# Kernel tuning notes

Measured on AMD Instinct MI355X. Metric: run time of the kernel, lower is better.

The kernel has to match this reference:

```python
import jax, jax.numpy as jnp
import numpy as np


def setup_inputs() -> dict:
    key = jax.random.key(0)
    k0, k1, k2, k3 = jax.random.split(key, 4)
    B, in_dim, n_vars, out_dim, E = 64, 512, 512, 720, 8
    x = jax.random.normal(k0, (B, in_dim, n_vars), dtype=jnp.float32)
    # Gating: nn.Linear(in_dim, E, bias=False) -> weight [E, in_dim]
    Wg = jax.random.normal(k1, (E, in_dim), dtype=jnp.float32) * 0.02
    # Experts: nn.Linear(in_dim, out_dim) -> weight [out_dim, in_dim], bias [out_dim]
    We = jax.random.normal(k2, (E, out_dim, in_dim), dtype=jnp.float32) * 0.02
    be = jax.random.normal(k3, (E, out_dim), dtype=jnp.float32) * 0.02
    return {"x": x, "Wg": Wg, "We": We, "be": be, "top_k": 2}


def reference(x, Wg, We, be, top_k):
    # x: [B, in_len, n_vars] -> tokens along n_vars with feature dim in_len
    xt = jnp.swapaxes(x, 1, 2)                      # [B, V, D]
    gate = jax.nn.softmax(xt @ Wg.T, axis=-1)       # [B, V, E]
    weights, sel = jax.lax.top_k(gate, top_k)       # [B, V, k]
    E, O, D = We.shape
    out = jnp.zeros(xt.shape[:2] + (O,), dtype=xt.dtype)  # [B, V, O]
    for e in range(E):
        # combine weight for expert e: sum over top-k slots routed to e
        coef = jnp.sum(jnp.where(sel == e, weights, jnp.zeros_like(weights)), axis=-1)  # [B, V]
        out = out + coef[..., None] * (jnp.einsum('bvd,od->bvo', xt, We[e]) + be[e])
    return jnp.swapaxes(out, 1, 2)                  # [B, pred_len, n_vars]
```

## Files before the change

### kernel.cpp

```cpp
#include <hip/hip_runtime.h>
#include <hip/hip_bf16.h>

#define DID 512
#define NV  512
#define NB  64
#define OD  720
#define OPAD 768
#define NE  8
#define NTOK (NB * NV)
#define MAXTILE 512

typedef short  bf16x8 __attribute__((ext_vector_type(8)));
typedef float  f32x4  __attribute__((ext_vector_type(4)));

#define XT_OFF    0u
#define WB_OFF    33554432u
#define PID_OFF   39845888u
#define C1D_OFF   39976960u
#define C2D_OFF   40108032u
#define TL_OFF    40239104u
#define CL1_OFF   40370176u
#define CL2_OFF   40501248u
#define BCNT_OFF  40632320u
#define BFILL_OFF 40632576u
#define BOFF_OFF  40632832u
#define TPID_OFF  40633088u
#define TT0_OFF   40635136u
#define TEND_OFF  40637184u
#define NT_OFF    40639232u
#define SCR_OFF   40639488u
#define SCR_END   87825408u

static __device__ __forceinline__ ushort f2bf(float f) {
  unsigned u = __float_as_uint(f);
  unsigned r = (u + 0x7fffu + ((u >> 16) & 1u)) >> 16;
  return (ushort)r;
}
static __device__ __forceinline__ float bf2f(ushort u) {
  return __uint_as_float(((unsigned)u) << 16);
}
static __device__ __forceinline__ void async16(const ushort* g, ushort* l) {
  __builtin_amdgcn_global_load_lds((__attribute__((address_space(1))) void*)(g),
                                   (__attribute__((address_space(3))) void*)(l),
                                   16, 0, 0);
}
static __device__ __forceinline__ int swz(int r) { return (r & 3) ^ ((r >> 2) & 1); }

__global__ __launch_bounds__(512) void k_gatet_wb(const float* __restrict__ x,
                                                  const float* __restrict__ Wg,
                                                  const float* __restrict__ We,
                                                  ushort* __restrict__ xt,
                                                  ushort* __restrict__ wb,
                                                  int* __restrict__ pairid,
                                                  float* __restrict__ c1d,
                                                  float* __restrict__ c2d,
                                                  int* __restrict__ bcnt) {
  const int bid = blockIdx.x;
  const int tid = threadIdx.x;

  if (bid >= 512) {
    const int idx = (bid - 512) * 512 + tid;
    const int e = idx / (OPAD * DID);
    const int r = idx - e * (OPAD * DID);
    const int o = r >> 9;
    ushort val = 0;
    if (o < OD) val = f2bf(We[(size_t)e * OD * DID + r]);
    wb[(size_t)e * OPAD * DID + idx - e * (OPAD * DID)] = val;
    return;
  }

  __shared__ float wg[NE * DID];
  __shared__ float part[8][64][NE + 1];
  __shared__ int cnt64[64];
  for (int i = tid; i < NE * DID / 4; i += 512)
    ((float4*)wg)[i] = ((const float4*)Wg)[i];
  if (tid < 64) cnt64[tid] = 0;
  __syncthreads();

  const int b    = bid >> 3;
  const int v0   = (bid & 7) * 64;
  const int w    = tid >> 6;
  const int lane = tid & 63;
  const int v    = v0 + lane;
  const int d0   = w * 64;
  const float* xp = x + ((size_t)b * DID + d0) * NV + v;
  ushort* xtp = xt + ((size_t)b * NV + v) * DID + d0;

  float acc[NE];
#pragma unroll
  for (int e = 0; e < NE; ++e) acc[e] = 0.f;

  for (int c = 0; c < 64; c += 8) {
    float xv[8];
#pragma unroll
    for (int u = 0; u < 8; ++u) xv[u] = xp[(size_t)(c + u) * NV];
#pragma unroll
    for (int e = 0; e < NE; ++e) {
      const float* wp = &wg[e * DID + d0 + c];
      float4 wa = *(const float4*)wp;
      float4 wb4 = *(const float4*)(wp + 4);
      acc[e] += xv[0] * wa.x + xv[1] * wa.y + xv[2] * wa.z + xv[3] * wa.w
              + xv[4] * wb4.x + xv[5] * wb4.y + xv[6] * wb4.z + xv[7] * wb4.w;
    }
    bf16x8 pk;
#pragma unroll
    for (int u = 0; u < 8; ++u) pk[u] = (short)f2bf(xv[u]);
    *(bf16x8*)(xtp + c) = pk;
  }

#pragma unroll
  for (int e = 0; e < NE; ++e) part[w][lane][e] = acc[e];
  __syncthreads();

  if (tid < 64) {
    float a[NE];
#pragma unroll
    for (int e = 0; e < NE; ++e) {
      float s = part[0][tid][e];
#pragma unroll
      for (int q = 1; q < 8; ++q) s += part[q][tid][e];
      a[e] = s;
    }
    float mx = a[0];
#pragma unroll
    for (int e = 1; e < NE; ++e) mx = fmaxf(mx, a[e]);
    float sum = 0.f;
#pragma unroll
    for (int e = 0; e < NE; ++e) { a[e] = __expf(a[e] - mx); sum += a[e]; }
    const float inv = 1.f / sum;

    int i1 = 0; float g1 = a[0];
#pragma unroll
    for (int e = 1; e < NE; ++e) if (a[e] > g1) { g1 = a[e]; i1 = e; }
    int i2 = -1; float g2 = -1.f;
#pragma unroll
    for (int e = 0; e < NE; ++e) if (e != i1 && a[e] > g2) { g2 = a[e]; i2 = e; }
    g1 *= inv; g2 *= inv;

    int ea, eb; float ca, cb;
    if (i1 < i2) { ea = i1; eb = i2; ca = g1; cb = g2; }
    else         { ea = i2; eb = i1; ca = g2; cb = g1; }
    const int pid = ea * 8 + eb;
    const int t = b * NV + v0 + tid;
    pairid[t] = pid; c1d[t] = ca; c2d[t] = cb;
    atomicAdd(&cnt64[pid], 1);
  }
  __syncthreads();
  if (tid < 64 && cnt64[tid]) atomicAdd(&bcnt[tid], cnt64[tid]);
}

__global__ __launch_bounds__(256) void k_scatter(const int* __restrict__ pairid,
                                                 const float* __restrict__ c1d,
                                                 const float* __restrict__ c2d,
                                                 const int* __restrict__ bcnt,
                                                 int* __restrict__ bfill,
                                                 int* __restrict__ tlist,
                                                 float* __restrict__ cl1,
                                                 float* __restrict__ cl2,
                                                 int* __restrict__ tpid,
                                                 int* __restrict__ tt0,
                                                 int* __restrict__ tend,
                                                 int* __restrict__ ntp) {
  __shared__ int cnt64[64], base64[64], boffl[64];
  const int tid = threadIdx.x;
  if (tid < 64) {
    const int c = bcnt[tid];
    int run = c;
#pragma unroll
    for (int s = 1; s < 64; s <<= 1) {
      int up = __shfl_up(run, s, 64);
      if (tid >= s) run += up;
    }
    const int excl = run - c;
    boffl[tid] = excl;
    cnt64[tid] = 0;
    if (blockIdx.x == 0) {
      const int ntiles = (c + 127) >> 7;
      int trun = ntiles;
#pragma unroll
      for (int s = 1; s < 64; s <<= 1) {
        int up = __shfl_up(trun, s, 64);
        if (tid >= s) trun += up;
      }
      const int texcl = trun - ntiles;
      for (int i = 0; i < ntiles; ++i) {
        tpid[texcl + i] = tid;
        tt0[texcl + i]  = excl + i * 128;
        tend[texcl + i] = run;
      }
      if (tid == 63) ntp[0] = trun;
    }
  }
  __syncthreads();
  const int t = blockIdx.x * 256 + tid;
  const int pid = pairid[t];
  const int p = atomicAdd(&cnt64[pid], 1);
  __syncthreads();
  if (tid < 64) base64[tid] = cnt64[tid] ? atomicAdd(&bfill[tid], cnt64[tid]) : 0;
  __syncthreads();
  const int slot = boffl[pid] + base64[pid] + p;
  tlist[slot] = t; cl1[slot] = c1d[t]; cl2[slot] = c2d[t];
}

__global__ __launch_bounds__(256, 2) void k_gemm(
    const ushort* __restrict__ xt, const ushort* __restrict__ wb,
    const float* __restrict__ be, const int* __restrict__ tlist,
    const float* __restrict__ cl1, const float* __restrict__ cl2,
    const int* __restrict__ tpid, const int* __restrict__ tt0,
    const int* __restrict__ tendarr, const int* __restrict__ ntp,
    ushort* __restrict__ scratch, float* __restrict__ out, int mode) {
  const int tile = blockIdx.x;
  if (tile >= ntp[0]) return;
  const int pid  = tpid[tile];
  const int t0   = tt0[tile];
  const int tend = tendarr[tile];
  const int e1 = pid >> 3, e2 = pid & 7;
  const int o0 = blockIdx.y * 256;

  __shared__ __align__(16) ushort As[3][8192];
  __shared__ __align__(16) ushort Bs[3][4096];

  const int tid  = threadIdx.x;
  const int lane = tid & 63;
  const int w    = tid >> 6;

  int aoffA[4];
#pragma unroll
  for (int i = 0; i < 4; ++i) {
    const int f = w * 256 + i * 64 + lane;
    const int r = f >> 2, p = f & 3, q = p ^ swz(r);
    aoffA[i] = (o0 + r) * DID + q * 8;
  }
  int boffB[2];
#pragma unroll
  for (int i = 0; i < 2; ++i) {
    const int f = w * 128 + i * 64 + lane;
    const int r = f >> 2, p = f & 3, q = p ^ swz(r);
    const int sl = t0 + r;
    const int tk = (sl < tend) ? tlist[sl] : 0;
    boffB[i] = tk * DID + q * 8;
  }

  const int m    = lane & 15;
  const int quad = lane >> 4;
  const int wt   = (w & 1) * 64;
  const int wo   = (w >> 1) * 128;

  float ratio[4], c2v[4]; int tokv[4]; bool gv[4];
#pragma unroll
  for (int j = 0; j < 4; ++j) {
    const int sl = t0 + wt + j * 16 + m;
    gv[j] = sl < tend;
    const float cc1 = gv[j] ? cl1[sl] : 0.f;
    const float cc2 = gv[j] ? cl2[sl] : 1.f;
    ratio[j] = cc1 / cc2;
    c2v[j]   = gv[j] ? cc2 : 0.f;
    tokv[j]  = gv[j] ? tlist[sl] : 0;
  }

  f32x4 acc[8][4];
#pragma unroll
  for (int i = 0; i < 8; ++i)
#pragma unroll
    for (int j = 0; j < 4; ++j) acc[i][j] = (f32x4){0.f, 0.f, 0.f, 0.f};

#define STAGE(t, buf) do {                                          \
    const int eA_ = ((t) < 16) ? e1 : e2;                           \
    const int k0_ = ((t) & 15) * 32;                                \
    const ushort* wA_ = wb + (size_t)eA_ * OPAD * DID + k0_;        \
    async16(wA_ + aoffA[0], &As[buf][w * 2048]);                    \
    async16(wA_ + aoffA[1], &As[buf][w * 2048 + 512]);              \
    async16(wA_ + aoffA[2], &As[buf][w * 2048 + 1024]);             \
    async16(wA_ + aoffA[3], &As[buf][w * 2048 + 1536]);             \
    async16(xt + boffB[0] + k0_, &Bs[buf][w * 1024]);               \
    async16(xt + boffB[1] + k0_, &Bs[buf][w * 1024 + 512]);         \
  } while (0)

#define FRAGS(buf)                                                       \
    bf16x8 af[8], bfr[4];                                                \
    {                                                                    \
      const ushort* Asb = &As[buf][0];                                   \
      const ushort* Bsb = &Bs[buf][0];                                   \
      _Pragma("unroll")                                                  \
      for (int i = 0; i < 8; ++i) {                                      \
        const int R = wo + i * 16 + m;                                   \
        af[i] = *(const bf16x8*)(Asb + R * 32 + ((quad ^ swz(R)) << 3)); \
      }                                                                  \
      _Pragma("unroll")                                                  \
      for (int j = 0; j < 4; ++j) {                                      \
        const int R = wt + j * 16 + m;                                   \
        bfr[j] = *(const bf16x8*)(Bsb + R * 32 + ((quad ^ swz(R)) << 3));\
      }                                                                  \
    }

#define MFMA32()                                                         \
    __builtin_amdgcn_s_setprio(1);                                       \
    _Pragma("unroll")                                                    \
    for (int i = 0; i < 8; ++i)                                          \
      _Pragma("unroll")                                                  \
      for (int j = 0; j < 4; ++j)                                        \
        acc[i][j] = __builtin_amdgcn_mfma_f32_16x16x32_bf16(af[i], bfr[j],\
                                                            acc[i][j], 0, 0, 0); \
    __builtin_amdgcn_s_setprio(0);

  STAGE(0, 0);
  STAGE(1, 1);

  int cur = 0;
  int st  = 2;
  for (int kk = 0; kk < 30; ++kk) {
    asm volatile("s_waitcnt vmcnt(6)" ::: "memory");
    __builtin_amdgcn_s_barrier();
    if (kk == 16) {
      const float* be1p = be + e1 * OD;
#pragma unroll
      for (int i = 0; i < 8; ++i) {
        const int ob = o0 + wo + i * 16 + quad * 4;
        float b0 = 0, b1 = 0, b2 = 0, b3 = 0;
        if (ob < OD) { b0 = be1p[ob]; b1 = be1p[ob + 1]; b2 = be1p[ob + 2]; b3 = be1p[ob + 3]; }
#pragma unroll
        for (int j = 0; j < 4; ++j) {
          acc[i][j][0] = (acc[i][j][0] + b0) * ratio[j];
          acc[i][j][1] = (acc[i][j][1] + b1) * ratio[j];
          acc[i][j][2] = (acc[i][j][2] + b2) * ratio[j];
          acc[i][j][3] = (acc[i][j][3] + b3) * ratio[j];
        }
      }
    }

    STAGE(kk + 2, st);
    FRAGS(cur)
    MFMA32()
    cur = (cur == 2) ? 0 : cur + 1;
    st  = (st  == 2) ? 0 : st  + 1;
  }

  {
    asm volatile("s_waitcnt vmcnt(6)" ::: "memory");
    __builtin_amdgcn_s_barrier();
    FRAGS(0)
    MFMA32()
  }
  {
    asm volatile("s_waitcnt vmcnt(0)" ::: "memory");
    __builtin_amdgcn_s_barrier();
    FRAGS(1)
    MFMA32()
  }

#undef STAGE
#undef FRAGS
#undef MFMA32

  const float* be2p = be + e2 * OD;
#pragma unroll
  for (int i = 0; i < 8; ++i) {
    const int ob = o0 + wo + i * 16 + quad * 4;
    if (ob < OD) {
      const float b0 = be2p[ob], b1 = be2p[ob + 1], b2 = be2p[ob + 2], b3 = be2p[ob + 3];
#pragma unroll
      for (int j = 0; j < 4; ++j) {
        if (gv[j]) {
          const float v0 = c2v[j] * (acc[i][j][0] + b0);
          const float v1 = c2v[j] * (acc[i][j][1] + b1);
          const float v2 = c2v[j] * (acc[i][j][2] + b2);
          const float v3 = c2v[j] * (acc[i][j][3] + b3);
          if (mode == 0) {
            ushort4 pk = make_ushort4(f2bf(v0), f2bf(v1), f2bf(v2), f2bf(v3));
            *(ushort4*)(scratch + (size_t)tokv[j] * OD + ob) = pk;
          } else {
            const int bb = tokv[j] >> 9, vv = tokv[j] & 511;
            float* op = out + ((size_t)bb * OD + ob) * NV + vv;
            op[0] = v0; op[(size_t)NV] = v1; op[2 * (size_t)NV] = v2; op[3 * (size_t)NV] = v3;
          }
        }
      }
    }
  }
}

__global__ __launch_bounds__(256) void k_combine(const ushort* __restrict__ scratch,
                                                 float* __restrict__ out) {
  __shared__ ushort s[64][68];
  const int v0 = blockIdx.x * 64;
  const int o0 = blockIdx.y * 64;
  const int b  = blockIdx.z;
  const int tid = threadIdx.x;
#pragma unroll
  for (int it = 0; it < 2; ++it) {
    const int c = it * 256 + tid;
    const int row = c >> 3, cg = c & 7;
    const int o = o0 + cg * 8;
    if (o + 8 <= OD) {
      const ushort* src = scratch + ((size_t)(b * NV + v0 + row)) * OD + o;
      ushort4 ua = *(const ushort4*)(src);
      ushort4 ub = *(const ushort4*)(src + 4);
      *(ushort4*)&s[row][cg * 8] = ua;
      *(ushort4*)&s[row][cg * 8 + 4] = ub;
    }
  }
  __syncthreads();
  const int vv = tid & 63;
  const int og = tid >> 6;
#pragma unroll
  for (int oi = 0; oi < 8; ++oi) {
    const int ol = (og * 8 + oi) * 2;
    const int o = o0 + ol;
    if (o < OD) {
      ushort2 u = *(const ushort2*)&s[vv][ol];
      float* op = out + ((size_t)b * OD + o) * NV + v0 + vv;
      op[0]  = bf2f(u.x);
      op[NV] = bf2f(u.y);
    }
  }
}

extern "C" void kernel_launch(void* const* d_in, const int* in_sizes, int n_in,
                              void* d_out, int out_size, void* d_ws, size_t ws_size,
                              hipStream_t stream) {
  const float* x  = (const float*)d_in[0];
  const float* Wg = (const float*)d_in[1];
  const float* We = (const float*)d_in[2];
  const float* be = (const float*)d_in[3];
  float* out = (float*)d_out;

  char* ws = (char*)d_ws;
  ushort* xt     = (ushort*)(ws + XT_OFF);
  ushort* wb     = (ushort*)(ws + WB_OFF);
  int*    pairid = (int*)   (ws + PID_OFF);
  float*  c1d    = (float*) (ws + C1D_OFF);
  float*  c2d    = (float*) (ws + C2D_OFF);
  int*    tlist  = (int*)   (ws + TL_OFF);
  float*  cl1    = (float*) (ws + CL1_OFF);
  float*  cl2    = (float*) (ws + CL2_OFF);
  int*    bcnt   = (int*)   (ws + BCNT_OFF);
  int*    bfill  = (int*)   (ws + BFILL_OFF);
  int*    tpid   = (int*)   (ws + TPID_OFF);
  int*    tt0    = (int*)   (ws + TT0_OFF);
  int*    tend   = (int*)   (ws + TEND_OFF);
  int*    ntp    = (int*)   (ws + NT_OFF);
  ushort* scratch= (ushort*)(ws + SCR_OFF);

  const int mode = (ws_size >= (size_t)SCR_END) ? 0 : 1;

  (void)hipMemsetAsync(bcnt, 0, 512, stream);

  k_gatet_wb<<<dim3(512 + NE * OPAD * DID / 512), 512, 0, stream>>>(
      x, Wg, We, xt, wb, pairid, c1d, c2d, bcnt);
  k_scatter<<<NTOK / 256, 256, 0, stream>>>(pairid, c1d, c2d, bcnt, bfill,
                                            tlist, cl1, cl2,
                                            tpid, tt0, tend, ntp);
  k_gemm<<<dim3(320, OPAD / 256), 256, 0, stream>>>(xt, wb, be, tlist, cl1, cl2,
                                                    tpid, tt0, tend, ntp,
                                                    scratch, out, mode);
  if (mode == 0)
    k_combine<<<dim3(NV / 64, (OD + 63) / 64, NB), 256, 0, stream>>>(scratch, out);
}
```

Before: 315.9 us.

## Load token operand directly from global into registers, deepen A pipeline to three stages

The gathered token (B) operand is no longer staged through LDS. Each lane reads its bf16x8 fragments straight from global memory through per-lane row pointers. This frees LDS, which lets the weight (A) tiles prefetch three stages ahead, with an extra barrier so a buffer is refilled only after it has been read. In exchange, B fragments become direct uncoalesced gathers of 16-byte chunks per k-step that sit on the MFMA critical path, and the added barrier per iteration may stall the waves.

```diff
diff --git a/kernel.cpp b/kernel.cpp
--- a/kernel.cpp
+++ b/kernel.cpp
@@ -65,7 +65,7 @@
     const int o = r >> 9;
     ushort val = 0;
     if (o < OD) val = f2bf(We[(size_t)e * OD * DID + r]);
-    wb[(size_t)e * OPAD * DID + idx - e * (OPAD * DID)] = val;
+    wb[(size_t)e * OPAD * DID + r] = val;
     return;
   }
 
@@ -218,7 +218,6 @@
   const int o0 = blockIdx.y * 256;
 
   __shared__ __align__(16) ushort As[3][8192];
-  __shared__ __align__(16) ushort Bs[3][4096];
 
   const int tid  = threadIdx.x;
   const int lane = tid & 63;
@@ -231,31 +230,24 @@
     const int r = f >> 2, p = f & 3, q = p ^ swz(r);
     aoffA[i] = (o0 + r) * DID + q * 8;
   }
-  int boffB[2];
-#pragma unroll
-  for (int i = 0; i < 2; ++i) {
-    const int f = w * 128 + i * 64 + lane;
-    const int r = f >> 2, p = f & 3, q = p ^ swz(r);
-    const int sl = t0 + r;
-    const int tk = (sl < tend) ? tlist[sl] : 0;
-    boffB[i] = tk * DID + q * 8;
-  }
 
   const int m    = lane & 15;
   const int quad = lane >> 4;
   const int wt   = (w & 1) * 64;
   const int wo   = (w >> 1) * 128;
 
-  float ratio[4], c2v[4]; int tokv[4]; bool gv[4];
+  float ratio[4], c2v[4];
+  const ushort* baddr[4];
 #pragma unroll
   for (int j = 0; j < 4; ++j) {
     const int sl = t0 + wt + j * 16 + m;
-    gv[j] = sl < tend;
-    const float cc1 = gv[j] ? cl1[sl] : 0.f;
-    const float cc2 = gv[j] ? cl2[sl] : 1.f;
+    const bool g = sl < tend;
+    const float cc1 = g ? cl1[sl] : 0.f;
+    const float cc2 = g ? cl2[sl] : 1.f;
     ratio[j] = cc1 / cc2;
-    c2v[j]   = gv[j] ? cc2 : 0.f;
-    tokv[j]  = gv[j] ? tlist[sl] : 0;
+    c2v[j]   = g ? cc2 : 0.f;
+    const int tk = g ? tlist[sl] : 0;
+    baddr[j] = xt + (size_t)tk * DID + quad * 8;
   }
 
   f32x4 acc[8][4];
@@ -272,24 +264,25 @@
     async16(wA_ + aoffA[1], &As[buf][w * 2048 + 512]);              \
     async16(wA_ + aoffA[2], &As[buf][w * 2048 + 1024]);             \
     async16(wA_ + aoffA[3], &As[buf][w * 2048 + 1536]);             \
-    async16(xt + boffB[0] + k0_, &Bs[buf][w * 1024]);               \
-    async16(xt + boffB[1] + k0_, &Bs[buf][w * 1024 + 512]);         \
   } while (0)
 
-#define FRAGS(buf)                                                       \
-    bf16x8 af[8], bfr[4];                                                \
+#define BLOAD(t)                                                         \
+    bf16x8 bfr[4];                                                       \
+    {                                                                    \
+      const int kt_ = ((t) & 15) * 32;                                   \
+      _Pragma("unroll")                                                  \
+      for (int j = 0; j < 4; ++j)                                        \
+        bfr[j] = *(const bf16x8*)(baddr[j] + kt_);                       \
+    }
+
+#define FRAGS_A(buf)                                                     \
+    bf16x8 af[8];                                                        \
     {                                                                    \
       const ushort* Asb = &As[buf][0];                                   \
-      const ushort* Bsb = &Bs[buf][0];                                   \
       _Pragma("unroll")                                                  \
       for (int i = 0; i < 8; ++i) {                                      \
         const int R = wo + i * 16 + m;                                   \
         af[i] = *(const bf16x8*)(Asb + R * 32 + ((quad ^ swz(R)) << 3)); \
-      }                                                                  \
-      _Pragma("unroll")                                                  \
-      for (int j = 0; j < 4; ++j) {                                      \
-        const int R = wt + j * 16 + m;                                   \
-        bfr[j] = *(const bf16x8*)(Bsb + R * 32 + ((quad ^ swz(R)) << 3));\
       }                                                                  \
     }
 
@@ -305,12 +298,13 @@
 
   STAGE(0, 0);
   STAGE(1, 1);
+  STAGE(2, 2);
 
   int cur = 0;
-  int st  = 2;
-  for (int kk = 0; kk < 30; ++kk) {
-    asm volatile("s_waitcnt vmcnt(6)" ::: "memory");
+  for (int kk = 0; kk < 29; ++kk) {
+    asm volatile("s_waitcnt vmcnt(8)" ::: "memory");
     __builtin_amdgcn_s_barrier();
+
     if (kk == 16) {
       const float* be1p = be + e1 * OD;
 #pragma unroll
@@ -328,28 +322,40 @@
       }
     }
 
-    STAGE(kk + 2, st);
-    FRAGS(cur)
+    BLOAD(kk)
+    FRAGS_A(cur)
+    asm volatile("s_waitcnt lgkmcnt(0)" ::: "memory");
+    __builtin_amdgcn_s_barrier();
+    STAGE(kk + 3, cur);
     MFMA32()
     cur = (cur == 2) ? 0 : cur + 1;
-    st  = (st  == 2) ? 0 : st  + 1;
   }
 
   {
-    asm volatile("s_waitcnt vmcnt(6)" ::: "memory");
+    asm volatile("s_waitcnt vmcnt(8)" ::: "memory");
     __builtin_amdgcn_s_barrier();
-    FRAGS(0)
+    BLOAD(29)
+    FRAGS_A(2)
+    MFMA32()
+  }
+  {
+    asm volatile("s_waitcnt vmcnt(4)" ::: "memory");
+    __builtin_amdgcn_s_barrier();
+    BLOAD(30)
+    FRAGS_A(0)
     MFMA32()
   }
   {
     asm volatile("s_waitcnt vmcnt(0)" ::: "memory");
     __builtin_amdgcn_s_barrier();
-    FRAGS(1)
+    BLOAD(31)
+    FRAGS_A(1)
     MFMA32()
   }
 
 #undef STAGE
-#undef FRAGS
+#undef BLOAD
+#undef FRAGS_A
 #undef MFMA32
 
   const float* be2p = be + e2 * OD;
@@ -360,16 +366,17 @@
       const float b0 = be2p[ob], b1 = be2p[ob + 1], b2 = be2p[ob + 2], b3 = be2p[ob + 3];
 #pragma unroll
       for (int j = 0; j < 4; ++j) {
-        if (gv[j]) {
+        if (c2v[j] != 0.f) {
+          const int tk = (int)(((size_t)(baddr[j] - xt)) >> 9);
           const float v0 = c2v[j] * (acc[i][j][0] + b0);
           const float v1 = c2v[j] * (acc[i][j][1] + b1);
           const float v2 = c2v[j] * (acc[i][j][2] + b2);
           const float v3 = c2v[j] * (acc[i][j][3] + b3);
           if (mode == 0) {
             ushort4 pk = make_ushort4(f2bf(v0), f2bf(v1), f2bf(v2), f2bf(v3));
-            *(ushort4*)(scratch + (size_t)tokv[j] * OD + ob) = pk;
+            *(ushort4*)(scratch + (size_t)tk * OD + ob) = pk;
           } else {
-            const int bb = tokv[j] >> 9, vv = tokv[j] & 511;
+            const int bb = tk >> 9, vv = tk & 511;
             float* op = out + ((size_t)bb * OD + ob) * NV + vv;
             op[0] = v0; op[(size_t)NV] = v1; op[2 * (size_t)NV] = v2; op[3 * (size_t)NV] = v3;
           }
```

New measurement: 335.5 us. +6.2%, slower.
